# Performance work log

Hardware: AMD Instinct MI355X
Metric: run time of the kernel (lower is better)

## Reference

```python
import jax, jax.numpy as jnp
import numpy as np

N = 50000        # nodes
E = 800000       # edges (avg degree 16)
NFEAT = 16       # 14 feat + 2 pos
NHID = 64
NCLASS = 1
NGRAPHS = 500
NLAYERS = 5
DT, ALPHA, GAMMA = 1.0, 1.0, 1.0


def _lin_init(k, fan_in, fan_out):
    # torch nn.Linear default: U(-1/sqrt(fan_in), 1/sqrt(fan_in))
    lim = 1.0 / np.sqrt(fan_in)
    kw, kb = jax.random.split(k)
    W = jax.random.uniform(kw, (fan_in, fan_out), minval=-lim, maxval=lim, dtype=jnp.float32)
    b = jax.random.uniform(kb, (fan_out,), minval=-lim, maxval=lim, dtype=jnp.float32)
    return W, b


def setup_inputs() -> dict:
    key = jax.random.key(0)
    ks = jax.random.split(key, 8)
    x = jax.random.normal(ks[0], (N, 14), dtype=jnp.float32)
    pos = jax.random.normal(ks[1], (N, 2), dtype=jnp.float32)
    edge_index = jax.random.randint(ks[2], (2, E), 0, N, dtype=jnp.int64)
    batch = jnp.sort(jax.random.randint(ks[3], (N,), 0, NGRAPHS, dtype=jnp.int64))
    enc_W, enc_b = _lin_init(ks[4], NFEAT, NHID)
    conv_W, conv_b = _lin_init(ks[5], NHID, NHID)
    res_W, res_b = _lin_init(ks[6], NHID, NHID)
    dec_W, dec_b = _lin_init(ks[7], NHID, NCLASS)
    return dict(x=x, pos=pos, edge_index=edge_index, batch=batch,
                enc_W=enc_W, enc_b=enc_b, conv_W=conv_W, conv_b=conv_b,
                res_W=res_W, res_b=res_b, dec_W=dec_W, dec_b=dec_b)


def _gcn_conv(h, src, dst, W, b):
    # PyG GCNConv: add self-loops, symmetric normalization, scatter-add to dst.
    loop = jnp.arange(N, dtype=src.dtype)
    src2 = jnp.concatenate([src, loop])
    dst2 = jnp.concatenate([dst, loop])
    deg = jax.ops.segment_sum(jnp.ones_like(dst2, dtype=h.dtype), dst2, num_segments=N)
    dinv = jnp.where(deg > 0, jax.lax.rsqrt(deg), 0.0)
    hW = h @ W                                   # [N, nhid]
    norm = dinv[src2] * dinv[dst2]               # [E+N]
    msg = hW[src2] * norm[:, None]               # [E+N, nhid]
    return jax.ops.segment_sum(msg, dst2, num_segments=N) + b


def reference(x, pos, edge_index, batch, enc_W, enc_b, conv_W, conv_b, res_W, res_b, dec_W, dec_b):
    src, dst = edge_index[0], edge_index[1]
    inp = jnp.concatenate([x, pos], axis=-1)     # [N, nfeat]
    Y = inp @ enc_W + enc_b
    X = Y
    # dropout p=0 -> identity (eval mode)
    for _ in range(NLAYERS):
        agg = _gcn_conv(X, src, dst, conv_W, conv_b) + (X @ res_W + res_b)
        Y = Y + DT * (jax.nn.relu(agg) - ALPHA * Y - GAMMA * X)
        X = X + DT * Y
    Xo = X @ dec_W + dec_b                       # [N, 1]
    pooled = jax.ops.segment_sum(Xo, batch, num_segments=NGRAPHS)  # [G, 1]
    return pooled.squeeze(-1)                    # [G]
```

## Files before the change

### kernel.cpp

```cpp
#include <hip/hip_runtime.h>

#define NN 50000
#define NE 800000
#define NH 64
#define NG 500
#define NPAD 50176
#define NBKT 782
#define CAP 1536

typedef __attribute__((ext_vector_type(8))) short bf16x8;
typedef __attribute__((ext_vector_type(4))) float f32x4;

__device__ __forceinline__ unsigned short f2bf(float f) {
  unsigned x = __float_as_uint(f);
  unsigned r = ((x >> 16) & 1u) + 0x7fffu;
  return (unsigned short)((x + r) >> 16);
}
__device__ __forceinline__ float bf2f(unsigned short u) {
  return __uint_as_float(((unsigned)u) << 16);
}


__global__ __launch_bounds__(256) void k_bin(const int* __restrict__ src, const int* __restrict__ dst,
                                             int* __restrict__ bcur, int* __restrict__ colp) {
  __shared__ int hist[NBKT];
  __shared__ int gbase[NBKT];
  int t = threadIdx.x;
  for (int b = t; b < NBKT; b += 256) hist[b] = 0;
  __syncthreads();
  int e0 = blockIdx.x * 8192;
#pragma unroll
  for (int i = 0; i < 32; i++) {
    int e = e0 + i * 256 + t;
    if (e < NE) atomicAdd(&hist[dst[e] >> 6], 1);
  }
  __syncthreads();
  for (int b = t; b < NBKT; b += 256) {
    int c = hist[b];
    gbase[b] = c ? atomicAdd(&bcur[b], c) : 0;
    hist[b] = 0;
  }
  __syncthreads();
#pragma unroll
  for (int i = 0; i < 32; i++) {
    int e = e0 + i * 256 + t;
    if (e < NE) {
      int s = src[e], d = dst[e];
      int b = d >> 6;
      int r = atomicAdd(&hist[b], 1);
      colp[b * CAP + gbase[b] + r] = (s << 6) | (d & 63);
    }
  }
}


__global__ __launch_bounds__(256) void k_csr(const int* __restrict__ bcur, const int* __restrict__ colp,
                                             int* __restrict__ cols, float* __restrict__ dinv,
                                             int* __restrict__ rowst, int* __restrict__ rowen,
                                             const int* __restrict__ batch, int* __restrict__ gptr) {
  __shared__ int hist[64];
  __shared__ int excl[65];
  int t = threadIdx.x;
  int b = blockIdx.x;

  int tid = b * 256 + t;
  if (tid < NN) {
    int bi = batch[tid];
    int bp = (tid > 0) ? batch[tid - 1] : -1;
    for (int g = bp + 1; g <= bi; g++) gptr[g] = tid;
    if (tid == NN - 1) {
      for (int g = bi + 1; g <= NG; g++) gptr[g] = NN;
    }
  }

  int base = b * CAP;
  int cnt = bcur[b];
  if (t < 64) hist[t] = 0;
  __syncthreads();
  for (int e = t; e < cnt; e += 256) atomicAdd(&hist[colp[base + e] & 63], 1);
  __syncthreads();
  if (t == 0) {
    int run = 0;
#pragma unroll
    for (int i = 0; i < 64; i++) { excl[i] = run; run += hist[i]; }
    excl[64] = run;
  }
  __syncthreads();
  if (t < 64) {
    int n = b * 64 + t;
    rowst[n] = base + excl[t];
    rowen[n] = base + excl[t + 1];
    if (n < NN) dinv[n] = rsqrtf((float)(hist[t] + 1));
    hist[t] = 0;
  }
  __syncthreads();
  for (int e = t; e < cnt; e += 256) {
    int w = colp[base + e];
    int d = w & 63;
    int r = atomicAdd(&hist[d], 1);
    cols[base + excl[d] + r] = w >> 6;
  }
}


__global__ __launch_bounds__(256) void k_encoder(const float* __restrict__ x, const float* __restrict__ pos,
                                                 const float* __restrict__ W, const float* __restrict__ b,
                                                 float* __restrict__ X0) {
  __shared__ float Ws[16 * 64];
  __shared__ float bs[64];
  int t = threadIdx.x;
  for (int i = t; i < 1024; i += 256) Ws[i] = W[i];
  if (t < 64) bs[t] = b[t];
  __syncthreads();
  int n = blockIdx.x * 4 + (t >> 6);
  int h = t & 63;
  if (n >= NN) return;
  float acc = bs[h];
#pragma unroll
  for (int f = 0; f < 14; f++) acc += x[n * 14 + f] * Ws[f * 64 + h];
  acc += pos[n * 2 + 0] * Ws[14 * 64 + h];
  acc += pos[n * 2 + 1] * Ws[15 * 64 + h];
  X0[n * 64 + h] = acc;
}


__global__ __launch_bounds__(256) void k_wprep(const float* __restrict__ Wc, const float* __restrict__ Wr,
                                               unsigned short* __restrict__ Wf) {
  int t = blockIdx.x * 256 + threadIdx.x;
  if (t >= 2048) return;
  int fid = t >> 6;
  int lane = t & 63;
  int ntile = fid & 3, s = (fid >> 2) & 1, part = (fid >> 3) & 1, mat = fid >> 4;
  const float* W = mat ? Wr : Wc;
  int col = ntile * 16 + (lane & 15);
  int k0 = s * 32 + (lane >> 4) * 8;
#pragma unroll
  for (int e = 0; e < 8; e++) {
    float w = W[(k0 + e) * 64 + col];
    unsigned short h = f2bf(w);
    Wf[(size_t)fid * 512 + lane * 8 + e] = part ? f2bf(w - bf2f(h)) : h;
  }
}


__global__ __launch_bounds__(256) void k_gemm_dual(const float* __restrict__ Xin,
                                                   const unsigned short* __restrict__ gsum,
                                                   const unsigned short* __restrict__ Wf,
                                                   const float* __restrict__ cb, const float* __restrict__ rb,
                                                   const float* __restrict__ dinv,
                                                   unsigned short* __restrict__ hWbf, float* __restrict__ agg,
                                                   int mode) {
  int lane = threadIdx.x & 63;
  int wv = threadIdx.x >> 6;
  int col16 = lane & 15;
  int kb = lane >> 4;
  int n0 = blockIdx.x * 64 + wv * 16;

  int nr = n0 + col16;
  int nc = nr < NN ? nr : NN - 1;
  const float* xrow = Xin + (size_t)nc * 64;
  float v0[8], v1[8];
  {
    float4 a = *(const float4*)(xrow + kb * 8);
    float4 b = *(const float4*)(xrow + kb * 8 + 4);
    float4 c = *(const float4*)(xrow + 32 + kb * 8);
    float4 d = *(const float4*)(xrow + 32 + kb * 8 + 4);
    v0[0] = a.x; v0[1] = a.y; v0[2] = a.z; v0[3] = a.w;
    v0[4] = b.x; v0[5] = b.y; v0[6] = b.z; v0[7] = b.w;
    v1[0] = c.x; v1[1] = c.y; v1[2] = c.z; v1[3] = c.w;
    v1[4] = d.x; v1[5] = d.y; v1[6] = d.z; v1[7] = d.w;
  }
  if (mode) {
    float dvn = dinv[nc];
    const unsigned* grow = (const unsigned*)(gsum + (size_t)nc * 64);
    uint4 g0 = *(const uint4*)(grow + kb * 4);
    uint4 g1 = *(const uint4*)(grow + 16 + kb * 4);
    unsigned ga[4] = {g0.x, g0.y, g0.z, g0.w};
    unsigned gb[4] = {g1.x, g1.y, g1.z, g1.w};
#pragma unroll
    for (int e = 0; e < 4; e++) {
      v0[2 * e]     = fmaxf(v0[2 * e]     + dvn * bf2f((unsigned short)(ga[e] & 0xffff)), 0.f);
      v0[2 * e + 1] = fmaxf(v0[2 * e + 1] + dvn * bf2f((unsigned short)(ga[e] >> 16)), 0.f);
      v1[2 * e]     = fmaxf(v1[2 * e]     + dvn * bf2f((unsigned short)(gb[e] & 0xffff)), 0.f);
      v1[2 * e + 1] = fmaxf(v1[2 * e + 1] + dvn * bf2f((unsigned short)(gb[e] >> 16)), 0.f);
    }
  }
  bf16x8 ah0, al0, ah1, al1;
#pragma unroll
  for (int e = 0; e < 8; e++) {
    unsigned short h0 = f2bf(v0[e]);
    ah0[e] = (short)h0;
    al0[e] = (short)f2bf(v0[e] - bf2f(h0));
    unsigned short h1 = f2bf(v1[e]);
    ah1[e] = (short)h1;
    al1[e] = (short)f2bf(v1[e] - bf2f(h1));
  }

  f32x4 aC[4] = {{0.f, 0.f, 0.f, 0.f}, {0.f, 0.f, 0.f, 0.f}, {0.f, 0.f, 0.f, 0.f}, {0.f, 0.f, 0.f, 0.f}};
  f32x4 aR[4] = {{0.f, 0.f, 0.f, 0.f}, {0.f, 0.f, 0.f, 0.f}, {0.f, 0.f, 0.f, 0.f}, {0.f, 0.f, 0.f, 0.f}};
  const bf16x8* WFv = (const bf16x8*)Wf;
#pragma unroll
  for (int j = 0; j < 4; j++) {
    bf16x8 wch0 = WFv[(j)      * 64 + lane];
    bf16x8 wch1 = WFv[(4 + j)  * 64 + lane];
    bf16x8 wcl0 = WFv[(8 + j)  * 64 + lane];
    bf16x8 wcl1 = WFv[(12 + j) * 64 + lane];
    bf16x8 wrh0 = WFv[(16 + j) * 64 + lane];
    bf16x8 wrh1 = WFv[(20 + j) * 64 + lane];
    bf16x8 wrl0 = WFv[(24 + j) * 64 + lane];
    bf16x8 wrl1 = WFv[(28 + j) * 64 + lane];
    f32x4 c = aC[j];
    c = __builtin_amdgcn_mfma_f32_16x16x32_bf16(ah0, wch0, c, 0, 0, 0);
    c = __builtin_amdgcn_mfma_f32_16x16x32_bf16(ah1, wch1, c, 0, 0, 0);
    c = __builtin_amdgcn_mfma_f32_16x16x32_bf16(al0, wch0, c, 0, 0, 0);
    c = __builtin_amdgcn_mfma_f32_16x16x32_bf16(al1, wch1, c, 0, 0, 0);
    c = __builtin_amdgcn_mfma_f32_16x16x32_bf16(ah0, wcl0, c, 0, 0, 0);
    c = __builtin_amdgcn_mfma_f32_16x16x32_bf16(ah1, wcl1, c, 0, 0, 0);
    aC[j] = c;
    f32x4 r = aR[j];
    r = __builtin_amdgcn_mfma_f32_16x16x32_bf16(ah0, wrh0, r, 0, 0, 0);
    r = __builtin_amdgcn_mfma_f32_16x16x32_bf16(ah1, wrh1, r, 0, 0, 0);
    r = __builtin_amdgcn_mfma_f32_16x16x32_bf16(al0, wrh0, r, 0, 0, 0);
    r = __builtin_amdgcn_mfma_f32_16x16x32_bf16(al1, wrh1, r, 0, 0, 0);
    r = __builtin_amdgcn_mfma_f32_16x16x32_bf16(ah0, wrl0, r, 0, 0, 0);
    r = __builtin_amdgcn_mfma_f32_16x16x32_bf16(ah1, wrl1, r, 0, 0, 0);
    aR[j] = r;
  }

  float cbv[4], rbv[4];
#pragma unroll
  for (int j = 0; j < 4; j++) { cbv[j] = cb[j * 16 + col16]; rbv[j] = rb[j * 16 + col16]; }
  int rbase = kb * 4;
#pragma unroll
  for (int r = 0; r < 4; r++) {
    int node = n0 + rbase + r;
    if (node < NN) {
      float dv = dinv[node];
      size_t o = (size_t)node * 64 + col16;
#pragma unroll
      for (int j = 0; j < 4; j++) {
        float hc = dv * aC[j][r];
        unsigned short hb = f2bf(hc);
        hWbf[o + j * 16] = hb;
        agg[o + j * 16] = aR[j][r] + rbv[j] + cbv[j] + dv * hc;
      }
    }
  }
}


__global__ __launch_bounds__(256) void k_gather(const int* __restrict__ rowst, const int* __restrict__ rowen,
                                                const int* __restrict__ cols,
                                                const unsigned short* __restrict__ hWbf,
                                                unsigned short* __restrict__ gsum,
                                                const float* __restrict__ agg, const float* __restrict__ dinv,
                                                const float* __restrict__ decW, float* __restrict__ Xo,
                                                int last) {
  int lane = threadIdx.x & 63;
  int h2 = lane & 31;
  int p = lane >> 5;
  int n = __builtin_amdgcn_readfirstlane(blockIdx.x * 4 + (threadIdx.x >> 6));
  int st = rowst[n];
  int en = rowen[n];
  int deg = en - st;
  float a0 = 0.f, a1 = 0.f;
  for (int base = 0; base < deg; base += 64) {
    int cnt = deg - base;
    if (cnt > 64) cnt = 64;
    int li = lane < cnt ? lane : cnt - 1;
    int colv = cols[st + base + li];
    for (int j = 0; j < cnt; j += 16) {
      int e0 = j + 0 + p, e1 = j + 2 + p, e2 = j + 4 + p, e3 = j + 6 + p;
      int e4 = j + 8 + p, e5 = j + 10 + p, e6 = j + 12 + p, e7 = j + 14 + p;
      int s0 = __shfl(colv, e0 < cnt ? e0 : j, 64);
      int s1 = __shfl(colv, e1 < cnt ? e1 : j, 64);
      int s2 = __shfl(colv, e2 < cnt ? e2 : j, 64);
      int s3 = __shfl(colv, e3 < cnt ? e3 : j, 64);
      int s4 = __shfl(colv, e4 < cnt ? e4 : j, 64);
      int s5 = __shfl(colv, e5 < cnt ? e5 : j, 64);
      int s6 = __shfl(colv, e6 < cnt ? e6 : j, 64);
      int s7 = __shfl(colv, e7 < cnt ? e7 : j, 64);
      unsigned u0 = *(const unsigned*)(hWbf + (size_t)s0 * 64 + h2 * 2);
      unsigned u1 = *(const unsigned*)(hWbf + (size_t)s1 * 64 + h2 * 2);
      unsigned u2 = *(const unsigned*)(hWbf + (size_t)s2 * 64 + h2 * 2);
      unsigned u3 = *(const unsigned*)(hWbf + (size_t)s3 * 64 + h2 * 2);
      unsigned u4 = *(const unsigned*)(hWbf + (size_t)s4 * 64 + h2 * 2);
      unsigned u5 = *(const unsigned*)(hWbf + (size_t)s5 * 64 + h2 * 2);
      unsigned u6 = *(const unsigned*)(hWbf + (size_t)s6 * 64 + h2 * 2);
      unsigned u7 = *(const unsigned*)(hWbf + (size_t)s7 * 64 + h2 * 2);
      a0 += (e0 < cnt) ? bf2f((unsigned short)(u0 & 0xffff)) : 0.f;
      a1 += (e0 < cnt) ? bf2f((unsigned short)(u0 >> 16)) : 0.f;
      a0 += (e1 < cnt) ? bf2f((unsigned short)(u1 & 0xffff)) : 0.f;
      a1 += (e1 < cnt) ? bf2f((unsigned short)(u1 >> 16)) : 0.f;
      a0 += (e2 < cnt) ? bf2f((unsigned short)(u2 & 0xffff)) : 0.f;
      a1 += (e2 < cnt) ? bf2f((unsigned short)(u2 >> 16)) : 0.f;
      a0 += (e3 < cnt) ? bf2f((unsigned short)(u3 & 0xffff)) : 0.f;
      a1 += (e3 < cnt) ? bf2f((unsigned short)(u3 >> 16)) : 0.f;
      a0 += (e4 < cnt) ? bf2f((unsigned short)(u4 & 0xffff)) : 0.f;
      a1 += (e4 < cnt) ? bf2f((unsigned short)(u4 >> 16)) : 0.f;
      a0 += (e5 < cnt) ? bf2f((unsigned short)(u5 & 0xffff)) : 0.f;
      a1 += (e5 < cnt) ? bf2f((unsigned short)(u5 >> 16)) : 0.f;
      a0 += (e6 < cnt) ? bf2f((unsigned short)(u6 & 0xffff)) : 0.f;
      a1 += (e6 < cnt) ? bf2f((unsigned short)(u6 >> 16)) : 0.f;
      a0 += (e7 < cnt) ? bf2f((unsigned short)(u7 & 0xffff)) : 0.f;
      a1 += (e7 < cnt) ? bf2f((unsigned short)(u7 >> 16)) : 0.f;
    }
  }
  a0 += __shfl_down(a0, 32, 64);
  a1 += __shfl_down(a1, 32, 64);
  if (!last) {
    if (lane < 32) {
      unsigned outw = (unsigned)f2bf(a0) | ((unsigned)f2bf(a1) << 16);
      *(unsigned*)(gsum + (size_t)n * 64 + h2 * 2) = outw;
    }
  } else {
    float dv = dinv[n];
    float2 ag = *(const float2*)(agg + (size_t)n * 64 + h2 * 2);
    float xf0 = ag.x + dv * a0;
    float xf1 = ag.y + dv * a1;
    float v = fmaxf(xf0, 0.f) * decW[h2 * 2] + fmaxf(xf1, 0.f) * decW[h2 * 2 + 1];
    v = (lane < 32) ? v : 0.f;
#pragma unroll
    for (int off = 32; off > 0; off >>= 1) v += __shfl_down(v, off, 64);
    if (lane == 0) Xo[n] = v;
  }
}


__global__ __launch_bounds__(256) void k_pool(const float* __restrict__ Xo, const int* __restrict__ gptr,
                                              const float* __restrict__ decb, float* __restrict__ out) {
  __shared__ float part[4];
  int g = blockIdx.x;
  int t = threadIdx.x;
  int st = gptr[g], en = gptr[g + 1];
  float v = 0.f;
  for (int i = st + t; i < en; i += 256) v += Xo[i];
#pragma unroll
  for (int off = 32; off > 0; off >>= 1) v += __shfl_down(v, off, 64);
  if ((t & 63) == 0) part[t >> 6] = v;
  __syncthreads();
  if (t == 0) out[g] = part[0] + part[1] + part[2] + part[3] + (float)(en - st) * decb[0];
}


extern "C" void kernel_launch(void* const* d_in, const int* in_sizes, int n_in,
                              void* d_out, int out_size, void* d_ws, size_t ws_size,
                              hipStream_t stream) {
  (void)in_sizes; (void)n_in; (void)out_size; (void)ws_size;
  const float* x     = (const float*)d_in[0];
  const float* pos   = (const float*)d_in[1];
  const int*   ei    = (const int*)d_in[2];
  const int*   batch = (const int*)d_in[3];
  const float* encW  = (const float*)d_in[4];
  const float* encb  = (const float*)d_in[5];
  const float* convW = (const float*)d_in[6];
  const float* convb = (const float*)d_in[7];
  const float* resW  = (const float*)d_in[8];
  const float* resb  = (const float*)d_in[9];
  const float* decW  = (const float*)d_in[10];
  const float* decb  = (const float*)d_in[11];
  float* out = (float*)d_out;

  const int* src = ei;
  const int* dst = ei + NE;

  float*          ws     = (float*)d_ws;
  float*          dinv   = ws;
  int*            rowst  = (int*)(ws + NPAD);
  int*            rowen  = (int*)(ws + 2 * NPAD);
  int*            bcur   = (int*)(ws + 3 * NPAD);
  int*            gptr   = bcur + 1024;
  float*          Xo     = (float*)(gptr + 512);
  int*            colp   = (int*)(Xo + NPAD);
  int*            cols   = colp + NBKT * CAP;
  unsigned short* hWbf   = (unsigned short*)(cols + NBKT * CAP);
  unsigned short* gsum   = hWbf + (size_t)NPAD * 64;
  float*          bufA   = (float*)(gsum + (size_t)NPAD * 64);
  float*          bufB   = bufA + NN * NH;
  unsigned short* Wf     = (unsigned short*)(bufB + NN * NH);

  hipMemsetAsync(bcur, 0, 1024 * sizeof(int), stream);

  k_wprep<<<8, 256, 0, stream>>>(convW, resW, Wf);
  k_bin<<<(NE + 8191) / 8192, 256, 0, stream>>>(src, dst, bcur, colp);
  k_csr<<<NBKT, 256, 0, stream>>>(bcur, colp, cols, dinv, rowst, rowen, batch, gptr);

  k_encoder<<<(NN + 3) / 4, 256, 0, stream>>>(x, pos, encW, encb, bufA);

  float* aggIn = bufA;
  float* aggOut = bufB;
  for (int l = 0; l < 5; l++) {
    int last = (l == 4) ? 1 : 0;
    k_gemm_dual<<<NBKT, 256, 0, stream>>>(aggIn, gsum, Wf, convb, resb, dinv,
                                          hWbf, aggOut, l > 0 ? 1 : 0);
    k_gather<<<NN / 4, 256, 0, stream>>>(rowst, rowen, cols, hWbf, gsum,
                                         aggOut, dinv, decW, Xo, last);
    float* tmp = aggIn; aggIn = aggOut; aggOut = tmp;
  }
  k_pool<<<NG, 256, 0, stream>>>(Xo, gptr, decb, out);
}
```

Measured before the change: 296.8 us.

## Fuse CSR build, encoder and gather with GEMM; pool via atomics

```diff
diff --git a/kernel.cpp b/kernel.cpp
--- a/kernel.cpp
+++ b/kernel.cpp
@@ -7,6 +7,7 @@
 #define NPAD 50176
 #define NBKT 782
 #define CAP 1536
+#define ZR NN
 
 typedef __attribute__((ext_vector_type(8))) short bf16x8;
 typedef __attribute__((ext_vector_type(4))) float f32x4;
@@ -18,6 +19,36 @@
 }
 __device__ __forceinline__ float bf2f(unsigned short u) {
   return __uint_as_float(((unsigned)u) << 16);
+}
+
+
+__global__ __launch_bounds__(256) void k_prep(const float* __restrict__ Wc, const float* __restrict__ Wr,
+                                              unsigned short* __restrict__ Wf,
+                                              int* __restrict__ bcur, float* __restrict__ out,
+                                              unsigned short* __restrict__ hWA, unsigned short* __restrict__ hWB) {
+  if (blockIdx.x == 8) {
+    int tt = threadIdx.x;
+    for (int i = tt; i < 1024; i += 256) bcur[i] = 0;
+    for (int i = tt; i < NG; i += 256) out[i] = 0.f;
+    if (tt < 32) {
+      ((unsigned*)(hWA + (size_t)ZR * 64))[tt] = 0u;
+      ((unsigned*)(hWB + (size_t)ZR * 64))[tt] = 0u;
+    }
+    return;
+  }
+  int t = blockIdx.x * 256 + threadIdx.x;
+  int fid = t >> 6;
+  int lane = t & 63;
+  int ntile = fid & 3, s = (fid >> 2) & 1, part = (fid >> 3) & 1, mat = fid >> 4;
+  const float* W = mat ? Wr : Wc;
+  int col = ntile * 16 + (lane & 15);
+  int k0 = s * 32 + (lane >> 4) * 8;
+#pragma unroll
+  for (int e = 0; e < 8; e++) {
+    float w = W[(k0 + e) * 64 + col];
+    unsigned short h = f2bf(w);
+    Wf[(size_t)fid * 512 + lane * 8 + e] = part ? f2bf(w - bf2f(h)) : h;
+  }
 }
 
 
@@ -54,123 +85,31 @@
 }
 
 
-__global__ __launch_bounds__(256) void k_csr(const int* __restrict__ bcur, const int* __restrict__ colp,
-                                             int* __restrict__ cols, float* __restrict__ dinv,
-                                             int* __restrict__ rowst, int* __restrict__ rowen,
-                                             const int* __restrict__ batch, int* __restrict__ gptr) {
-  __shared__ int hist[64];
-  __shared__ int excl[65];
-  int t = threadIdx.x;
-  int b = blockIdx.x;
-
-  int tid = b * 256 + t;
-  if (tid < NN) {
-    int bi = batch[tid];
-    int bp = (tid > 0) ? batch[tid - 1] : -1;
-    for (int g = bp + 1; g <= bi; g++) gptr[g] = tid;
-    if (tid == NN - 1) {
-      for (int g = bi + 1; g <= NG; g++) gptr[g] = NN;
-    }
-  }
-
-  int base = b * CAP;
-  int cnt = bcur[b];
-  if (t < 64) hist[t] = 0;
-  __syncthreads();
-  for (int e = t; e < cnt; e += 256) atomicAdd(&hist[colp[base + e] & 63], 1);
-  __syncthreads();
-  if (t == 0) {
-    int run = 0;
-#pragma unroll
-    for (int i = 0; i < 64; i++) { excl[i] = run; run += hist[i]; }
-    excl[64] = run;
-  }
-  __syncthreads();
-  if (t < 64) {
-    int n = b * 64 + t;
-    rowst[n] = base + excl[t];
-    rowen[n] = base + excl[t + 1];
-    if (n < NN) dinv[n] = rsqrtf((float)(hist[t] + 1));
-    hist[t] = 0;
-  }
-  __syncthreads();
-  for (int e = t; e < cnt; e += 256) {
-    int w = colp[base + e];
-    int d = w & 63;
-    int r = atomicAdd(&hist[d], 1);
-    cols[base + excl[d] + r] = w >> 6;
-  }
-}
-
-
-__global__ __launch_bounds__(256) void k_encoder(const float* __restrict__ x, const float* __restrict__ pos,
-                                                 const float* __restrict__ W, const float* __restrict__ b,
-                                                 float* __restrict__ X0) {
-  __shared__ float Ws[16 * 64];
-  __shared__ float bs[64];
-  int t = threadIdx.x;
-  for (int i = t; i < 1024; i += 256) Ws[i] = W[i];
-  if (t < 64) bs[t] = b[t];
-  __syncthreads();
-  int n = blockIdx.x * 4 + (t >> 6);
-  int h = t & 63;
-  if (n >= NN) return;
-  float acc = bs[h];
-#pragma unroll
-  for (int f = 0; f < 14; f++) acc += x[n * 14 + f] * Ws[f * 64 + h];
-  acc += pos[n * 2 + 0] * Ws[14 * 64 + h];
-  acc += pos[n * 2 + 1] * Ws[15 * 64 + h];
-  X0[n * 64 + h] = acc;
-}
-
-
-__global__ __launch_bounds__(256) void k_wprep(const float* __restrict__ Wc, const float* __restrict__ Wr,
-                                               unsigned short* __restrict__ Wf) {
-  int t = blockIdx.x * 256 + threadIdx.x;
-  if (t >= 2048) return;
-  int fid = t >> 6;
-  int lane = t & 63;
-  int ntile = fid & 3, s = (fid >> 2) & 1, part = (fid >> 3) & 1, mat = fid >> 4;
-  const float* W = mat ? Wr : Wc;
-  int col = ntile * 16 + (lane & 15);
-  int k0 = s * 32 + (lane >> 4) * 8;
-#pragma unroll
-  for (int e = 0; e < 8; e++) {
-    float w = W[(k0 + e) * 64 + col];
-    unsigned short h = f2bf(w);
-    Wf[(size_t)fid * 512 + lane * 8 + e] = part ? f2bf(w - bf2f(h)) : h;
-  }
-}
-
-
-__global__ __launch_bounds__(256) void k_gemm_dual(const float* __restrict__ Xin,
-                                                   const unsigned short* __restrict__ gsum,
-                                                   const unsigned short* __restrict__ Wf,
-                                                   const float* __restrict__ cb, const float* __restrict__ rb,
-                                                   const float* __restrict__ dinv,
-                                                   unsigned short* __restrict__ hWbf, float* __restrict__ agg,
-                                                   int mode) {
-  int lane = threadIdx.x & 63;
-  int wv = threadIdx.x >> 6;
+template <int NJT, int MODE>
+__device__ __forceinline__ void gemm_tile(int lane, int n0, int jbase,
+                                          const float* __restrict__ Xin,
+                                          const unsigned short* __restrict__ gsum,
+                                          const unsigned short* __restrict__ Wf,
+                                          const float* __restrict__ cb, const float* __restrict__ rb,
+                                          const float* __restrict__ dinv,
+                                          unsigned short* __restrict__ hWout, float* __restrict__ agg) {
   int col16 = lane & 15;
   int kb = lane >> 4;
-  int n0 = blockIdx.x * 64 + wv * 16;
-
   int nr = n0 + col16;
   int nc = nr < NN ? nr : NN - 1;
   const float* xrow = Xin + (size_t)nc * 64;
   float v0[8], v1[8];
   {
     float4 a = *(const float4*)(xrow + kb * 8);
-    float4 b = *(const float4*)(xrow + kb * 8 + 4);
+    float4 b4 = *(const float4*)(xrow + kb * 8 + 4);
     float4 c = *(const float4*)(xrow + 32 + kb * 8);
     float4 d = *(const float4*)(xrow + 32 + kb * 8 + 4);
     v0[0] = a.x; v0[1] = a.y; v0[2] = a.z; v0[3] = a.w;
-    v0[4] = b.x; v0[5] = b.y; v0[6] = b.z; v0[7] = b.w;
+    v0[4] = b4.x; v0[5] = b4.y; v0[6] = b4.z; v0[7] = b4.w;
     v1[0] = c.x; v1[1] = c.y; v1[2] = c.z; v1[3] = c.w;
     v1[4] = d.x; v1[5] = d.y; v1[6] = d.z; v1[7] = d.w;
   }
-  if (mode) {
+  if (MODE) {
     float dvn = dinv[nc];
     const unsigned* grow = (const unsigned*)(gsum + (size_t)nc * 64);
     uint4 g0 = *(const uint4*)(grow + kb * 4);
@@ -196,19 +135,24 @@
     al1[e] = (short)f2bf(v1[e] - bf2f(h1));
   }
 
-  f32x4 aC[4] = {{0.f, 0.f, 0.f, 0.f}, {0.f, 0.f, 0.f, 0.f}, {0.f, 0.f, 0.f, 0.f}, {0.f, 0.f, 0.f, 0.f}};
-  f32x4 aR[4] = {{0.f, 0.f, 0.f, 0.f}, {0.f, 0.f, 0.f, 0.f}, {0.f, 0.f, 0.f, 0.f}, {0.f, 0.f, 0.f, 0.f}};
+  f32x4 aC[NJT], aR[NJT];
+#pragma unroll
+  for (int j = 0; j < NJT; j++) {
+    aC[j] = (f32x4){0.f, 0.f, 0.f, 0.f};
+    aR[j] = (f32x4){0.f, 0.f, 0.f, 0.f};
+  }
   const bf16x8* WFv = (const bf16x8*)Wf;
 #pragma unroll
-  for (int j = 0; j < 4; j++) {
-    bf16x8 wch0 = WFv[(j)      * 64 + lane];
-    bf16x8 wch1 = WFv[(4 + j)  * 64 + lane];
-    bf16x8 wcl0 = WFv[(8 + j)  * 64 + lane];
-    bf16x8 wcl1 = WFv[(12 + j) * 64 + lane];
-    bf16x8 wrh0 = WFv[(16 + j) * 64 + lane];
-    bf16x8 wrh1 = WFv[(20 + j) * 64 + lane];
-    bf16x8 wrl0 = WFv[(24 + j) * 64 + lane];
-    bf16x8 wrl1 = WFv[(28 + j) * 64 + lane];
+  for (int j = 0; j < NJT; j++) {
+    int jj = jbase + j;
+    bf16x8 wch0 = WFv[(jj)      * 64 + lane];
+    bf16x8 wch1 = WFv[(4 + jj)  * 64 + lane];
+    bf16x8 wcl0 = WFv[(8 + jj)  * 64 + lane];
+    bf16x8 wcl1 = WFv[(12 + jj) * 64 + lane];
+    bf16x8 wrh0 = WFv[(16 + jj) * 64 + lane];
+    bf16x8 wrh1 = WFv[(20 + jj) * 64 + lane];
+    bf16x8 wrl0 = WFv[(24 + jj) * 64 + lane];
+    bf16x8 wrl1 = WFv[(28 + jj) * 64 + lane];
     f32x4 c = aC[j];
     c = __builtin_amdgcn_mfma_f32_16x16x32_bf16(ah0, wch0, c, 0, 0, 0);
     c = __builtin_amdgcn_mfma_f32_16x16x32_bf16(ah1, wch1, c, 0, 0, 0);
@@ -227,9 +171,12 @@
     aR[j] = r;
   }
 
-  float cbv[4], rbv[4];
-#pragma unroll
-  for (int j = 0; j < 4; j++) { cbv[j] = cb[j * 16 + col16]; rbv[j] = rb[j * 16 + col16]; }
+  float cbv[NJT], rbv[NJT];
+#pragma unroll
+  for (int j = 0; j < NJT; j++) {
+    cbv[j] = cb[(jbase + j) * 16 + col16];
+    rbv[j] = rb[(jbase + j) * 16 + col16];
+  }
   int rbase = kb * 4;
 #pragma unroll
   for (int r = 0; r < 4; r++) {
@@ -238,108 +185,178 @@
       float dv = dinv[node];
       size_t o = (size_t)node * 64 + col16;
 #pragma unroll
-      for (int j = 0; j < 4; j++) {
+      for (int j = 0; j < NJT; j++) {
+        int jj = jbase + j;
         float hc = dv * aC[j][r];
         unsigned short hb = f2bf(hc);
-        hWbf[o + j * 16] = hb;
-        agg[o + j * 16] = aR[j][r] + rbv[j] + cbv[j] + dv * hc;
+        hWout[o + jj * 16] = hb;
+        agg[o + jj * 16] = aR[j][r] + rbv[j] + cbv[j] + dv * hc;
       }
     }
   }
 }
 
 
-__global__ __launch_bounds__(256) void k_gather(const int* __restrict__ rowst, const int* __restrict__ rowen,
-                                                const int* __restrict__ cols,
-                                                const unsigned short* __restrict__ hWbf,
-                                                unsigned short* __restrict__ gsum,
-                                                const float* __restrict__ agg, const float* __restrict__ dinv,
-                                                const float* __restrict__ decW, float* __restrict__ Xo,
-                                                int last) {
-  int lane = threadIdx.x & 63;
+__global__ __launch_bounds__(256) void k_csr_enc_g0(const int* __restrict__ bcur, const int* __restrict__ colp,
+                                                    int* __restrict__ cols, float* __restrict__ dinv,
+                                                    int* __restrict__ rowst, int* __restrict__ rowen,
+                                                    const float* __restrict__ x, const float* __restrict__ pos,
+                                                    const float* __restrict__ encW, const float* __restrict__ encb,
+                                                    const unsigned short* __restrict__ Wf,
+                                                    const float* __restrict__ cb, const float* __restrict__ rb,
+                                                    unsigned short* __restrict__ hWout,
+                                                    float* __restrict__ X0, float* __restrict__ agg) {
+  __shared__ int hist[64];
+  __shared__ int excl[65];
+  __shared__ float Ws[16 * 64];
+  __shared__ float bs[64];
+  int t = threadIdx.x;
+  int b = blockIdx.x;
+
+  for (int i = t; i < 1024; i += 256) Ws[i] = encW[i];
+  if (t < 64) bs[t] = encb[t];
+
+  int base = b * CAP;
+  int cnt = bcur[b];
+  if (t < 64) hist[t] = 0;
+  __syncthreads();
+  for (int e = t; e < cnt; e += 256) atomicAdd(&hist[colp[base + e] & 63], 1);
+  __syncthreads();
+  if (t == 0) {
+    int run = 0;
+#pragma unroll
+    for (int i = 0; i < 64; i++) { excl[i] = run; run += hist[i]; }
+    excl[64] = run;
+  }
+  __syncthreads();
+  if (t < 64) {
+    int n = b * 64 + t;
+    rowst[n] = base + excl[t];
+    rowen[n] = base + excl[t + 1];
+    if (n < NN) dinv[n] = rsqrtf((float)(hist[t] + 1));
+    hist[t] = 0;
+  }
+  __syncthreads();
+  for (int e = t; e < cnt; e += 256) {
+    int w = colp[base + e];
+    int d = w & 63;
+    int r = atomicAdd(&hist[d], 1);
+    cols[base + excl[d] + r] = w >> 6;
+  }
+
+  int h = t & 63;
+  int nset = t >> 6;
+#pragma unroll
+  for (int i = 0; i < 16; i++) {
+    int n = b * 64 + nset * 16 + i;
+    if (n < NN) {
+      const float* xr = x + n * 14;
+      float acc = bs[h];
+#pragma unroll
+      for (int f = 0; f < 14; f++) acc += xr[f] * Ws[f * 64 + h];
+      acc += pos[n * 2 + 0] * Ws[14 * 64 + h];
+      acc += pos[n * 2 + 1] * Ws[15 * 64 + h];
+      X0[(size_t)n * 64 + h] = acc;
+    }
+  }
+  __syncthreads();
+
+  int lane = t & 63;
+  int wv = t >> 6;
+  gemm_tile<4, 0>(lane, b * 64 + wv * 16, 0, X0, (const unsigned short*)0, Wf, cb, rb, dinv, hWout, agg);
+}
+
+
+#define GSTEP(K)                                          \
+  {                                                       \
+    int e = j + 2 * (K) + p;                              \
+    int s = __shfl(colv, e, 64);                          \
+    s = e < cnt ? s : ZR;                                 \
+    unsigned u = hW32[(unsigned)s * 32u + (unsigned)h2];  \
+    a0 += __uint_as_float(u << 16);                       \
+    a1 += __uint_as_float(u & 0xffff0000u);               \
+  }
+
+
+__global__ __launch_bounds__(512) void k_gather_gemm(const int* __restrict__ rowst, const int* __restrict__ rowen,
+                                                     const int* __restrict__ cols,
+                                                     const unsigned short* __restrict__ hWin,
+                                                     unsigned short* __restrict__ hWout,
+                                                     unsigned short* __restrict__ gsum,
+                                                     const unsigned short* __restrict__ Wf,
+                                                     const float* __restrict__ cb, const float* __restrict__ rb,
+                                                     const float* __restrict__ dinv,
+                                                     const float* __restrict__ aggIn, float* __restrict__ aggOut) {
+  int t = threadIdx.x;
+  int lane = t & 63;
+  int wv = t >> 6;
+  int b = blockIdx.x;
   int h2 = lane & 31;
   int p = lane >> 5;
-  int n = __builtin_amdgcn_readfirstlane(blockIdx.x * 4 + (threadIdx.x >> 6));
+  const unsigned* __restrict__ hW32 = (const unsigned*)hWin;
+  unsigned* __restrict__ gs32 = (unsigned*)gsum;
+
+#pragma unroll 2
+  for (int i = 0; i < 8; i++) {
+    int n = __builtin_amdgcn_readfirstlane(b * 64 + wv * 8 + i);
+    int st = rowst[n];
+    int en = rowen[n];
+    int deg = en - st;
+    float a0 = 0.f, a1 = 0.f;
+    for (int base2 = 0; base2 < deg; base2 += 64) {
+      int cnt = deg - base2;
+      if (cnt > 64) cnt = 64;
+      int li = lane < cnt ? lane : cnt - 1;
+      int colv = cols[st + base2 + li];
+      for (int j = 0; j < cnt; j += 16) {
+        GSTEP(0) GSTEP(1) GSTEP(2) GSTEP(3) GSTEP(4) GSTEP(5) GSTEP(6) GSTEP(7)
+      }
+    }
+    a0 += __shfl_down(a0, 32, 64);
+    a1 += __shfl_down(a1, 32, 64);
+    if (lane < 32) gs32[(unsigned)n * 32u + (unsigned)h2] = (unsigned)f2bf(a0) | ((unsigned)f2bf(a1) << 16);
+  }
+  __syncthreads();
+
+  int rt = wv >> 1, ch = wv & 1;
+  gemm_tile<2, 1>(lane, b * 64 + rt * 16, ch * 2, aggIn, gsum, Wf, cb, rb, dinv, hWout, aggOut);
+}
+
+
+__global__ __launch_bounds__(256) void k_gather_final(const int* __restrict__ rowst, const int* __restrict__ rowen,
+                                                      const int* __restrict__ cols,
+                                                      const unsigned short* __restrict__ hWin,
+                                                      const float* __restrict__ aggIn, const float* __restrict__ dinv,
+                                                      const float* __restrict__ decW, const float* __restrict__ decb,
+                                                      const int* __restrict__ batch, float* __restrict__ out) {
+  int t = threadIdx.x;
+  int lane = t & 63;
+  int h2 = lane & 31;
+  int p = lane >> 5;
+  int n = __builtin_amdgcn_readfirstlane(blockIdx.x * 4 + (t >> 6));
+  const unsigned* __restrict__ hW32 = (const unsigned*)hWin;
   int st = rowst[n];
   int en = rowen[n];
   int deg = en - st;
   float a0 = 0.f, a1 = 0.f;
-  for (int base = 0; base < deg; base += 64) {
-    int cnt = deg - base;
+  for (int base2 = 0; base2 < deg; base2 += 64) {
+    int cnt = deg - base2;
     if (cnt > 64) cnt = 64;
     int li = lane < cnt ? lane : cnt - 1;
-    int colv = cols[st + base + li];
+    int colv = cols[st + base2 + li];
     for (int j = 0; j < cnt; j += 16) {
-      int e0 = j + 0 + p, e1 = j + 2 + p, e2 = j + 4 + p, e3 = j + 6 + p;
-      int e4 = j + 8 + p, e5 = j + 10 + p, e6 = j + 12 + p, e7 = j + 14 + p;
-      int s0 = __shfl(colv, e0 < cnt ? e0 : j, 64);
-      int s1 = __shfl(colv, e1 < cnt ? e1 : j, 64);
-      int s2 = __shfl(colv, e2 < cnt ? e2 : j, 64);
-      int s3 = __shfl(colv, e3 < cnt ? e3 : j, 64);
-      int s4 = __shfl(colv, e4 < cnt ? e4 : j, 64);
-      int s5 = __shfl(colv, e5 < cnt ? e5 : j, 64);
-      int s6 = __shfl(colv, e6 < cnt ? e6 : j, 64);
-      int s7 = __shfl(colv, e7 < cnt ? e7 : j, 64);
-      unsigned u0 = *(const unsigned*)(hWbf + (size_t)s0 * 64 + h2 * 2);
-      unsigned u1 = *(const unsigned*)(hWbf + (size_t)s1 * 64 + h2 * 2);
-      unsigned u2 = *(const unsigned*)(hWbf + (size_t)s2 * 64 + h2 * 2);
-      unsigned u3 = *(const unsigned*)(hWbf + (size_t)s3 * 64 + h2 * 2);
-      unsigned u4 = *(const unsigned*)(hWbf + (size_t)s4 * 64 + h2 * 2);
-      unsigned u5 = *(const unsigned*)(hWbf + (size_t)s5 * 64 + h2 * 2);
-      unsigned u6 = *(const unsigned*)(hWbf + (size_t)s6 * 64 + h2 * 2);
-      unsigned u7 = *(const unsigned*)(hWbf + (size_t)s7 * 64 + h2 * 2);
-      a0 += (e0 < cnt) ? bf2f((unsigned short)(u0 & 0xffff)) : 0.f;
-      a1 += (e0 < cnt) ? bf2f((unsigned short)(u0 >> 16)) : 0.f;
-      a0 += (e1 < cnt) ? bf2f((unsigned short)(u1 & 0xffff)) : 0.f;
-      a1 += (e1 < cnt) ? bf2f((unsigned short)(u1 >> 16)) : 0.f;
-      a0 += (e2 < cnt) ? bf2f((unsigned short)(u2 & 0xffff)) : 0.f;
-      a1 += (e2 < cnt) ? bf2f((unsigned short)(u2 >> 16)) : 0.f;
-      a0 += (e3 < cnt) ? bf2f((unsigned short)(u3 & 0xffff)) : 0.f;
-      a1 += (e3 < cnt) ? bf2f((unsigned short)(u3 >> 16)) : 0.f;
-      a0 += (e4 < cnt) ? bf2f((unsigned short)(u4 & 0xffff)) : 0.f;
-      a1 += (e4 < cnt) ? bf2f((unsigned short)(u4 >> 16)) : 0.f;
-      a0 += (e5 < cnt) ? bf2f((unsigned short)(u5 & 0xffff)) : 0.f;
-      a1 += (e5 < cnt) ? bf2f((unsigned short)(u5 >> 16)) : 0.f;
-      a0 += (e6 < cnt) ? bf2f((unsigned short)(u6 & 0xffff)) : 0.f;
-      a1 += (e6 < cnt) ? bf2f((unsigned short)(u6 >> 16)) : 0.f;
-      a0 += (e7 < cnt) ? bf2f((unsigned short)(u7 & 0xffff)) : 0.f;
-      a1 += (e7 < cnt) ? bf2f((unsigned short)(u7 >> 16)) : 0.f;
+      GSTEP(0) GSTEP(1) GSTEP(2) GSTEP(3) GSTEP(4) GSTEP(5) GSTEP(6) GSTEP(7)
     }
   }
   a0 += __shfl_down(a0, 32, 64);
   a1 += __shfl_down(a1, 32, 64);
-  if (!last) {
-    if (lane < 32) {
-      unsigned outw = (unsigned)f2bf(a0) | ((unsigned)f2bf(a1) << 16);
-      *(unsigned*)(gsum + (size_t)n * 64 + h2 * 2) = outw;
-    }
-  } else {
-    float dv = dinv[n];
-    float2 ag = *(const float2*)(agg + (size_t)n * 64 + h2 * 2);
-    float xf0 = ag.x + dv * a0;
-    float xf1 = ag.y + dv * a1;
-    float v = fmaxf(xf0, 0.f) * decW[h2 * 2] + fmaxf(xf1, 0.f) * decW[h2 * 2 + 1];
-    v = (lane < 32) ? v : 0.f;
-#pragma unroll
-    for (int off = 32; off > 0; off >>= 1) v += __shfl_down(v, off, 64);
-    if (lane == 0) Xo[n] = v;
-  }
-}
-
-
-__global__ __launch_bounds__(256) void k_pool(const float* __restrict__ Xo, const int* __restrict__ gptr,
-                                              const float* __restrict__ decb, float* __restrict__ out) {
-  __shared__ float part[4];
-  int g = blockIdx.x;
-  int t = threadIdx.x;
-  int st = gptr[g], en = gptr[g + 1];
-  float v = 0.f;
-  for (int i = st + t; i < en; i += 256) v += Xo[i];
+  float dv = dinv[n];
+  float2 ag = *(const float2*)(aggIn + (size_t)n * 64 + h2 * 2);
+  float v = fmaxf(ag.x + dv * a0, 0.f) * decW[h2 * 2] + fmaxf(ag.y + dv * a1, 0.f) * decW[h2 * 2 + 1];
+  v = (lane < 32) ? v : 0.f;
 #pragma unroll
   for (int off = 32; off > 0; off >>= 1) v += __shfl_down(v, off, 64);
-  if ((t & 63) == 0) part[t >> 6] = v;
-  __syncthreads();
-  if (t == 0) out[g] = part[0] + part[1] + part[2] + part[3] + (float)(en - st) * decb[0];
+  if (lane == 0) atomicAdd(&out[batch[n]], v + decb[0]);
 }
 
 
@@ -364,38 +381,28 @@
   const int* src = ei;
   const int* dst = ei + NE;
 
-  float*          ws     = (float*)d_ws;
-  float*          dinv   = ws;
-  int*            rowst  = (int*)(ws + NPAD);
-  int*            rowen  = (int*)(ws + 2 * NPAD);
-  int*            bcur   = (int*)(ws + 3 * NPAD);
-  int*            gptr   = bcur + 1024;
-  float*          Xo     = (float*)(gptr + 512);
-  int*            colp   = (int*)(Xo + NPAD);
-  int*            cols   = colp + NBKT * CAP;
-  unsigned short* hWbf   = (unsigned short*)(cols + NBKT * CAP);
-  unsigned short* gsum   = hWbf + (size_t)NPAD * 64;
-  float*          bufA   = (float*)(gsum + (size_t)NPAD * 64);
-  float*          bufB   = bufA + NN * NH;
-  unsigned short* Wf     = (unsigned short*)(bufB + NN * NH);
-
-  hipMemsetAsync(bcur, 0, 1024 * sizeof(int), stream);
-
-  k_wprep<<<8, 256, 0, stream>>>(convW, resW, Wf);
+  float*          ws    = (float*)d_ws;
+  float*          dinv  = ws;
+  int*            rowst = (int*)(ws + NPAD);
+  int*            rowen = (int*)(ws + 2 * NPAD);
+  int*            bcur  = (int*)(ws + 3 * NPAD);
+  int*            colp  = bcur + 1024;
+  int*            cols  = colp + NBKT * CAP;
+  unsigned short* hWA   = (unsigned short*)(cols + NBKT * CAP);
+  unsigned short* hWB   = hWA + (size_t)NPAD * 64;
+  unsigned short* gsum  = hWB + (size_t)NPAD * 64;
+  float*          bufA  = (float*)(gsum + (size_t)NPAD * 64);
+  float*          bufB  = bufA + NN * NH;
+  unsigned short* Wf    = (unsigned short*)(bufB + NN * NH);
+
+  k_prep<<<9, 256, 0, stream>>>(convW, resW, Wf, bcur, out, hWA, hWB);
   k_bin<<<(NE + 8191) / 8192, 256, 0, stream>>>(src, dst, bcur, colp);
-  k_csr<<<NBKT, 256, 0, stream>>>(bcur, colp, cols, dinv, rowst, rowen, batch, gptr);
-
-  k_encoder<<<(NN + 3) / 4, 256, 0, stream>>>(x, pos, encW, encb, bufA);
-
-  float* aggIn = bufA;
-  float* aggOut = bufB;
-  for (int l = 0; l < 5; l++) {
-    int last = (l == 4) ? 1 : 0;
-    k_gemm_dual<<<NBKT, 256, 0, stream>>>(aggIn, gsum, Wf, convb, resb, dinv,
-                                          hWbf, aggOut, l > 0 ? 1 : 0);
-    k_gather<<<NN / 4, 256, 0, stream>>>(rowst, rowen, cols, hWbf, gsum,
-                                         aggOut, dinv, decW, Xo, last);
-    float* tmp = aggIn; aggIn = aggOut; aggOut = tmp;
-  }
-  k_pool<<<NG, 256, 0, stream>>>(Xo, gptr, decb, out);
-}
+  k_csr_enc_g0<<<NBKT, 256, 0, stream>>>(bcur, colp, cols, dinv, rowst, rowen,
+                                         x, pos, encW, encb, Wf, convb, resb,
+                                         hWA, bufA, bufB);
+  k_gather_gemm<<<NBKT, 512, 0, stream>>>(rowst, rowen, cols, hWA, hWB, gsum, Wf, convb, resb, dinv, bufB, bufA);
+  k_gather_gemm<<<NBKT, 512, 0, stream>>>(rowst, rowen, cols, hWB, hWA, gsum, Wf, convb, resb, dinv, bufA, bufB);
+  k_gather_gemm<<<NBKT, 512, 0, stream>>>(rowst, rowen, cols, hWA, hWB, gsum, Wf, convb, resb, dinv, bufB, bufA);
+  k_gather_gemm<<<NBKT, 512, 0, stream>>>(rowst, rowen, cols, hWB, hWA, gsum, Wf, convb, resb, dinv, bufA, bufB);
+  k_gather_final<<<NN / 4, 256, 0, stream>>>(rowst, rowen, cols, hWA, bufB, dinv, decW, decb, batch, out);
+}
```

Result: slower. 347.7 us (+17.2%).
